# Optimization experiments

Hardware: AMD Instinct MI355X
Metric: run time of the kernel (lower is better)

## Reference

```python
import jax, jax.numpy as jnp
import numpy as np

N_HEAD = 12

def fillnan(x):
    return jnp.nan_to_num(x, nan=0.0, posinf=0.0, neginf=0.0)

def setup_inputs() -> dict:
    key = jax.random.key(0)
    k1, k2, k3 = jax.random.split(key, 3)
    B, T, C = 2, 2048, 768
    x = jax.random.normal(k1, (B, T, C), dtype=jnp.float32)
    W_attn = jax.random.normal(k2, (3 * C, C), dtype=jnp.float32) * 0.02
    W_proj = jax.random.normal(k3, (C, C), dtype=jnp.float32) * 0.02
    return {"x": x, "W_attn": W_attn, "W_proj": W_proj}

def reference(x, W_attn, W_proj):
    B, T, C = x.shape
    H = N_HEAD
    D = C // H
    # qkv projection (torch Linear: x @ W^T), then nan-sanitize
    qkv = fillnan(jnp.einsum('btc,fc->btf', x, W_attn))  # [B,T,3C]
    q, k, v = jnp.split(qkv, 3, axis=-1)
    # [B,T,C] -> [B,H,T,D]
    q = q.reshape(B, T, H, D).transpose(0, 2, 1, 3)
    k = k.reshape(B, T, H, D).transpose(0, 2, 1, 3)
    v = v.reshape(B, T, H, D).transpose(0, 2, 1, 3)
    scale = 1.0 / np.sqrt(D).astype(np.float32)
    att = jnp.einsum('bhqd,bhkd->bhqk', q, k) * scale  # [B,H,T,T]
    att = fillnan(att)
    causal = jnp.tril(jnp.ones((T, T), dtype=bool))
    att = jnp.where(causal[None, None], att, -jnp.inf)
    att = jax.nn.softmax(att, axis=-1)
    att = fillnan(att)
    y = jnp.einsum('bhqk,bhkd->bhqd', att, v)  # [B,H,T,D]
    y = fillnan(y)
    y = y.transpose(0, 2, 1, 3).reshape(B, T, C)
    y = fillnan(jnp.einsum('btc,fc->btf', y, W_proj))
    return y
```

## Files before the change

kernel.cpp:

```cpp
#include <hip/hip_runtime.h>

typedef __attribute__((ext_vector_type(8))) short bf16x8;
typedef __attribute__((ext_vector_type(4))) float f32x4;

__device__ __forceinline__ unsigned short f2b(float f) {
  union { float f; unsigned u; } v; v.f = f;
  return (unsigned short)((v.u + 0x7FFFu + ((v.u >> 16) & 1u)) >> 16);
}
__device__ __forceinline__ unsigned short f2b_fast(float f) {
  union { float f; unsigned u; } v; v.f = f;
  return (unsigned short)((v.u + 0x8000u) >> 16);
}

#define XN4   786432
#define WAN4  442368
#define WPN4  147456
__global__ void cvt_all(const float* __restrict__ x, const float* __restrict__ Wa,
                        const float* __restrict__ Wp,
                        unsigned short* __restrict__ xb, unsigned short* __restrict__ Wab,
                        unsigned short* __restrict__ Wpb) {
  int i = blockIdx.x * 256 + threadIdx.x;
  const float* src; unsigned short* dst; int off;
  if (i < XN4)            { src = x;  dst = xb;  off = i; }
  else if (i < XN4 + WAN4){ src = Wa; dst = Wab; off = i - XN4; }
  else                    { src = Wp; dst = Wpb; off = i - XN4 - WAN4; }
  float4 f = reinterpret_cast<const float4*>(src)[off];
  ushort4 o;
  o.x = f2b(f.x); o.y = f2b(f.y); o.z = f2b(f.z); o.w = f2b(f.w);
  reinterpret_cast<ushort4*>(dst)[off] = o;
}

#define BM 128
#define BN 128
#define BK 64

__global__ __launch_bounds__(256, 2)
void gemm_nt(const unsigned short* __restrict__ A,
             const unsigned short* __restrict__ Bm,
             int M, int N, int K, int mode,
             unsigned short* __restrict__ qb,
             unsigned short* __restrict__ kb_,
             unsigned short* __restrict__ vt,
             float* __restrict__ outf) {
  __shared__ unsigned short As[BM * BK];
  __shared__ unsigned short Bs[BN * BK];
  int tid = threadIdx.x;
  int wave = tid >> 6, lane = tid & 63;
  int quad = lane >> 4, l16 = lane & 15;
  int m0 = blockIdx.x * BM, n0 = blockIdx.y * BN;
  int wm = (wave & 1) * 64, wn = (wave >> 1) * 64;

  int srow = lane >> 3;
  int scol = ((lane & 7) ^ srow) << 3;

  f32x4 acc[4][4] = {};

  for (int k0 = 0; k0 < K; k0 += BK) {
    __syncthreads();
#pragma unroll
    for (int i = 0; i < 4; ++i) {
      int r = wave * 32 + i * 8;
      __builtin_amdgcn_global_load_lds(
          (const __attribute__((address_space(1))) unsigned int*)(A + (size_t)(m0 + r + srow) * K + k0 + scol),
          (__attribute__((address_space(3))) unsigned int*)(As + r * BK), 16, 0, 0);
      __builtin_amdgcn_global_load_lds(
          (const __attribute__((address_space(1))) unsigned int*)(Bm + (size_t)(n0 + r + srow) * K + k0 + scol),
          (__attribute__((address_space(3))) unsigned int*)(Bs + r * BK), 16, 0, 0);
    }
    __syncthreads();
#pragma unroll
    for (int kb = 0; kb < 2; ++kb) {
      int ch = (((kb << 2) | quad) ^ (l16 & 7)) << 3;
      bf16x8 af[4], bf[4];
#pragma unroll
      for (int i = 0; i < 4; ++i)
        af[i] = *reinterpret_cast<const bf16x8*>(As + (wm + i * 16 + l16) * BK + ch);
#pragma unroll
      for (int j = 0; j < 4; ++j)
        bf[j] = *reinterpret_cast<const bf16x8*>(Bs + (wn + j * 16 + l16) * BK + ch);
#pragma unroll
      for (int i = 0; i < 4; ++i)
#pragma unroll
        for (int j = 0; j < 4; ++j)
          acc[i][j] = __builtin_amdgcn_mfma_f32_16x16x32_bf16(af[i], bf[j], acc[i][j], 0, 0, 0);
    }
  }

  const float scale2 = 0.125f * 1.44269504089f;
#pragma unroll
  for (int i = 0; i < 4; ++i) {
    int mbase = m0 + wm + i * 16 + quad * 4;
#pragma unroll
    for (int j = 0; j < 4; ++j) {
      int f = n0 + wn + j * 16 + l16;
#pragma unroll
      for (int r = 0; r < 4; ++r) {
        float c = acc[i][j][r];
        int m = mbase + r;
        if (mode == 0) {
          int b = m >> 11, t = m & 2047;
          int which = f / 768;
          int f2 = f - which * 768;
          int h = f2 >> 6, d = f2 & 63;
          int bh = b * 12 + h;
          if (which == 0)      qb[((size_t)(bh * 2048 + t)) * 64 + d] = f2b(c * scale2);
          else if (which == 1) kb_[((size_t)(bh * 2048 + t)) * 64 + d] = f2b(c);
          else                 vt[((size_t)(bh * 64 + d)) * 2048 + t] = f2b(c);
        } else {
          outf[(size_t)m * N + f] = c;
        }
      }
    }
  }
}

#define PLDP 72

__global__ __launch_bounds__(256, 2)
void attn_part(const unsigned short* __restrict__ Qb,
               const unsigned short* __restrict__ Kb,
               const unsigned short* __restrict__ Vt,
               unsigned short* __restrict__ Yb) {
  __shared__ unsigned short Ks[2][64 * 64];
  __shared__ unsigned short Vs[2][64 * 64];
  __shared__ unsigned short P[4 * 32 * PLDP];
  const int T = 2048, D = 64;
  int wave = threadIdx.x >> 6, lane = threadIdx.x & 63;
  int quad = lane >> 4, l16 = lane & 15;

  int bh = blockIdx.x % 24;
  int qb = 15 - blockIdx.x / 24;
  int q0 = qb * 128;
  int qrow = q0 + wave * 32;
  int nt = 2 * qb + 2;

  const unsigned short* Qp = Qb + (size_t)bh * T * D;
  const unsigned short* Kp = Kb + (size_t)bh * T * D;
  const unsigned short* Vp = Vt + (size_t)bh * D * T;
  unsigned short* Pw = P + wave * 32 * PLDP;

  int srow = lane >> 3;
  int scol = ((lane & 7) ^ srow) << 3;

  bf16x8 aq[2][2];
#pragma unroll
  for (int qi = 0; qi < 2; ++qi)
#pragma unroll
    for (int cc = 0; cc < 2; ++cc)
      aq[qi][cc] = *reinterpret_cast<const bf16x8*>(
          Qp + (qrow + qi * 16 + l16) * D + cc * 32 + quad * 8);

  bf16x8 ones;
#pragma unroll
  for (int e = 0; e < 8; ++e) ones[e] = (short)0x3F80;

  f32x4 o[2][4] = {};
  f32x4 lacc[2] = {};

#define STAGE_KV(buf, k0s)                                                          \
  {                                                                                 \
    _Pragma("unroll")                                                               \
    for (int i_ = 0; i_ < 2; ++i_) {                                                \
      int rr_ = wave * 16 + i_ * 8;                                                 \
      __builtin_amdgcn_global_load_lds(                                             \
          (const __attribute__((address_space(1))) unsigned int*)(Kp + (size_t)((k0s) + rr_ + srow) * 64 + scol), \
          (__attribute__((address_space(3))) unsigned int*)(&Ks[buf][rr_ * 64]), 16, 0, 0); \
      __builtin_amdgcn_global_load_lds(                                             \
          (const __attribute__((address_space(1))) unsigned int*)(Vp + (size_t)(rr_ + srow) * 2048 + (k0s) + scol), \
          (__attribute__((address_space(3))) unsigned int*)(&Vs[buf][rr_ * 64]), 16, 0, 0); \
    }                                                                               \
  }

  STAGE_KV(0, 0);
  asm volatile("s_waitcnt vmcnt(0)" ::: "memory");
  __builtin_amdgcn_s_barrier();

  int cur = 0;
  for (int t = 0; t < nt; ++t) {
    int k0 = t << 6;
    if (t + 1 < nt) STAGE_KV(cur ^ 1, (t + 1) << 6);

    if (k0 <= qrow + 31) {
      f32x4 sacc[2][4] = {};
      __builtin_amdgcn_s_setprio(1);
#pragma unroll
      for (int nt2 = 0; nt2 < 4; ++nt2) {
        bf16x8 bk0 = *reinterpret_cast<const bf16x8*>(Ks[cur] + (nt2 * 16 + l16) * 64 + ((quad ^ (l16 & 7)) << 3));
        bf16x8 bk1 = *reinterpret_cast<const bf16x8*>(Ks[cur] + (nt2 * 16 + l16) * 64 + (((4 | quad) ^ (l16 & 7)) << 3));
#pragma unroll
        for (int qi = 0; qi < 2; ++qi) {
          sacc[qi][nt2] = __builtin_amdgcn_mfma_f32_16x16x32_bf16(aq[qi][0], bk0, sacc[qi][nt2], 0, 0, 0);
          sacc[qi][nt2] = __builtin_amdgcn_mfma_f32_16x16x32_bf16(aq[qi][1], bk1, sacc[qi][nt2], 0, 0, 0);
        }
      }
      __builtin_amdgcn_s_setprio(0);

      if (k0 + 63 > qrow) {
#pragma unroll
        for (int qi = 0; qi < 2; ++qi)
#pragma unroll
          for (int nt2 = 0; nt2 < 4; ++nt2) {
            int col = k0 + nt2 * 16 + l16;
#pragma unroll
            for (int rr = 0; rr < 4; ++rr) {
              int row = qrow + qi * 16 + quad * 4 + rr;
              sacc[qi][nt2][rr] = (col <= row) ? sacc[qi][nt2][rr] : -1e30f;
            }
          }
      }
#pragma unroll
      for (int qi = 0; qi < 2; ++qi)
#pragma unroll
        for (int nt2 = 0; nt2 < 4; ++nt2)
#pragma unroll
          for (int rr = 0; rr < 4; ++rr)
            sacc[qi][nt2][rr] = exp2f(sacc[qi][nt2][rr]);

#pragma unroll
      for (int qi = 0; qi < 2; ++qi)
#pragma unroll
        for (int nt2 = 0; nt2 < 4; ++nt2)
#pragma unroll
          for (int rr = 0; rr < 4; ++rr)
            Pw[(qi * 16 + quad * 4 + rr) * PLDP + nt2 * 16 + l16] = f2b_fast(sacc[qi][nt2][rr]);
      __asm__ volatile("s_waitcnt lgkmcnt(0)" ::: "memory");

      bf16x8 vf[4][2];
#pragma unroll
      for (int dt = 0; dt < 4; ++dt) {
        vf[dt][0] = *reinterpret_cast<const bf16x8*>(Vs[cur] + (dt * 16 + l16) * 64 + ((quad ^ (l16 & 7)) << 3));
        vf[dt][1] = *reinterpret_cast<const bf16x8*>(Vs[cur] + (dt * 16 + l16) * 64 + (((4 | quad) ^ (l16 & 7)) << 3));
      }
      __builtin_amdgcn_s_setprio(1);
#pragma unroll
      for (int qi = 0; qi < 2; ++qi) {
        bf16x8 ap0 = *reinterpret_cast<const bf16x8*>(Pw + (qi * 16 + l16) * PLDP + quad * 8);
        bf16x8 ap1 = *reinterpret_cast<const bf16x8*>(Pw + (qi * 16 + l16) * PLDP + 32 + quad * 8);
#pragma unroll
        for (int dt = 0; dt < 4; ++dt) {
          o[qi][dt] = __builtin_amdgcn_mfma_f32_16x16x32_bf16(ap0, vf[dt][0], o[qi][dt], 0, 0, 0);
          o[qi][dt] = __builtin_amdgcn_mfma_f32_16x16x32_bf16(ap1, vf[dt][1], o[qi][dt], 0, 0, 0);
        }
        lacc[qi] = __builtin_amdgcn_mfma_f32_16x16x32_bf16(ap0, ones, lacc[qi], 0, 0, 0);
        lacc[qi] = __builtin_amdgcn_mfma_f32_16x16x32_bf16(ap1, ones, lacc[qi], 0, 0, 0);
      }
      __builtin_amdgcn_s_setprio(0);
    }

    asm volatile("s_waitcnt vmcnt(0)" ::: "memory");
    __builtin_amdgcn_s_barrier();
    cur ^= 1;
  }

  int b = bh / 12, h = bh - b * 12;
  unsigned short* Yw = Yb + (size_t)b * 2048 * 768 + h * 64;
#pragma unroll
  for (int qi = 0; qi < 2; ++qi)
#pragma unroll
    for (int rr = 0; rr < 4; ++rr) {
      int row = qrow + qi * 16 + quad * 4 + rr;
      float rl = 1.0f / lacc[qi][rr];
#pragma unroll
      for (int dt = 0; dt < 4; ++dt)
        Yw[(size_t)row * 768 + dt * 16 + l16] = f2b(o[qi][dt][rr] * rl);
    }
}

extern "C" void kernel_launch(void* const* d_in, const int* in_sizes, int n_in,
                              void* d_out, int out_size, void* d_ws, size_t ws_size,
                              hipStream_t stream) {
  const float* x  = (const float*)d_in[0];
  const float* Wa = (const float*)d_in[1];
  const float* Wp = (const float*)d_in[2];
  float* out = (float*)d_out;

  unsigned short* ws = (unsigned short*)d_ws;
  unsigned short* xb  = ws;
  unsigned short* Wab = xb  + 3145728;
  unsigned short* Wpb = Wab + 1769472;
  unsigned short* Qb  = Wpb + 589824;
  unsigned short* Kb  = Qb  + 3145728;
  unsigned short* Vt  = Kb  + 3145728;
  unsigned short* Yb  = Vt  + 3145728;

  cvt_all<<<(XN4 + WAN4 + WPN4) / 256, 256, 0, stream>>>(x, Wa, Wp, xb, Wab, Wpb);

  gemm_nt<<<dim3(4096 / BM, 2304 / BN), 256, 0, stream>>>(
      xb, Wab, 4096, 2304, 768, 0, Qb, Kb, Vt, nullptr);

  attn_part<<<384, 256, 0, stream>>>(Qb, Kb, Vt, Yb);

  gemm_nt<<<dim3(4096 / BM, 768 / BN), 256, 0, stream>>>(
      Yb, Wpb, 4096, 768, 768, 1, nullptr, nullptr, nullptr, out);
}
```

Before: 166.2 us.

## Split causal attention along KV into balanced chunks with separate combine kernel

Each query block's KV range is now split into a number of chunks that grows with its causal length, so the grid goes from 384 to 960 more evenly sized blocks. Partial unnormalized outputs and row sums are written to fp32 workspace, and a new combine kernel sums them and normalizes into bf16 Y. Occupancy hint is raised to 3 blocks per CU. The aim is less tail imbalance from the causal triangle and better CU fill; the cost is extra fp32 partial-output traffic and one more kernel launch. Summing partials without rescaling assumes the softmax uses no per-row running max, which appears to hold in the existing code.

```diff
diff --git a/kernel.cpp b/kernel.cpp
--- a/kernel.cpp
+++ b/kernel.cpp
@@ -116,11 +116,11 @@
 
 #define PLDP 72
 
-__global__ __launch_bounds__(256, 2)
+__global__ __launch_bounds__(256, 3)
 void attn_part(const unsigned short* __restrict__ Qb,
                const unsigned short* __restrict__ Kb,
                const unsigned short* __restrict__ Vt,
-               unsigned short* __restrict__ Yb) {
+               float* __restrict__ Opart, float* __restrict__ Lpart) {
   __shared__ unsigned short Ks[2][64 * 64];
   __shared__ unsigned short Vs[2][64 * 64];
   __shared__ unsigned short P[4 * 32 * PLDP];
@@ -128,11 +128,20 @@
   int wave = threadIdx.x >> 6, lane = threadIdx.x & 63;
   int quad = lane >> 4, l16 = lane & 15;
 
-  int bh = blockIdx.x % 24;
-  int qb = 15 - blockIdx.x / 24;
+  int w = blockIdx.x;
+  int bh = w / 40;
+  int r = 39 - (w - bh * 40);
+  int qb, ci;
+  if (r < 4)       { qb = r;                 ci = 0; }
+  else if (r < 12) { qb = 4 + ((r - 4) >> 1);  ci = (r - 4) & 1; }
+  else if (r < 24) { qb = 8 + (r - 12) / 3;    ci = (r - 12) % 3; }
+  else             { qb = 12 + ((r - 24) >> 2); ci = (r - 24) & 3; }
+  int nk = 2 * qb + 2;
+  int nc = (qb >> 2) + 1;
+  int t0 = ci * nk / nc, t1 = (ci + 1) * nk / nc;
+
   int q0 = qb * 128;
   int qrow = q0 + wave * 32;
-  int nt = 2 * qb + 2;
 
   const unsigned short* Qp = Qb + (size_t)bh * T * D;
   const unsigned short* Kp = Kb + (size_t)bh * T * D;
@@ -171,14 +180,14 @@
     }                                                                               \
   }
 
-  STAGE_KV(0, 0);
+  STAGE_KV(0, t0 << 6);
   asm volatile("s_waitcnt vmcnt(0)" ::: "memory");
   __builtin_amdgcn_s_barrier();
 
   int cur = 0;
-  for (int t = 0; t < nt; ++t) {
+  for (int t = t0; t < t1; ++t) {
     int k0 = t << 6;
-    if (t + 1 < nt) STAGE_KV(cur ^ 1, (t + 1) << 6);
+    if (t + 1 < t1) STAGE_KV(cur ^ 1, (t + 1) << 6);
 
     if (k0 <= qrow + 31) {
       f32x4 sacc[2][4] = {};
@@ -252,18 +261,51 @@
     cur ^= 1;
   }
 
+  float* Op = Opart + (size_t)blockIdx.x * 8192 + wave * 32 * 64;
+#pragma unroll
+  for (int qi = 0; qi < 2; ++qi)
+#pragma unroll
+    for (int dt = 0; dt < 4; ++dt)
+#pragma unroll
+      for (int rr = 0; rr < 4; ++rr)
+        Op[(qi * 16 + quad * 4 + rr) * 64 + dt * 16 + l16] = o[qi][dt][rr];
+  if (l16 == 0) {
+#pragma unroll
+    for (int qi = 0; qi < 2; ++qi)
+#pragma unroll
+      for (int rr = 0; rr < 4; ++rr)
+        Lpart[blockIdx.x * 128 + wave * 32 + qi * 16 + quad * 4 + rr] = lacc[qi][rr];
+  }
+}
+
+__global__ __launch_bounds__(256)
+void attn_combine(const float* __restrict__ Opart, const float* __restrict__ Lpart,
+                  unsigned short* __restrict__ Yb) {
+  int blk = blockIdx.x;
+  int bh = blk >> 4, qb = blk & 15;
+  int off = (qb < 4) ? qb : (qb < 8) ? 4 + 2 * (qb - 4)
+          : (qb < 12) ? 12 + 3 * (qb - 8) : 24 + 4 * (qb - 12);
+  int nc = (qb >> 2) + 1;
   int b = bh / 12, h = bh - b * 12;
-  unsigned short* Yw = Yb + (size_t)b * 2048 * 768 + h * 64;
-#pragma unroll
-  for (int qi = 0; qi < 2; ++qi)
-#pragma unroll
-    for (int rr = 0; rr < 4; ++rr) {
-      int row = qrow + qi * 16 + quad * 4 + rr;
-      float rl = 1.0f / lacc[qi][rr];
-#pragma unroll
-      for (int dt = 0; dt < 4; ++dt)
-        Yw[(size_t)row * 768 + dt * 16 + l16] = f2b(o[qi][dt][rr] * rl);
-    }
+  int q0 = qb * 128;
+#pragma unroll
+  for (int i = 0; i < 8; ++i) {
+    int idx = i * 256 + threadIdx.x;
+    int row = idx >> 4, c4 = idx & 15;
+    float4 s = {0.f, 0.f, 0.f, 0.f};
+    float L = 0.f;
+    for (int ci = 0; ci < nc; ++ci) {
+      size_t pb = (size_t)(bh * 40 + 39 - (off + ci));
+      float4 v = *reinterpret_cast<const float4*>(Opart + pb * 8192 + row * 64 + c4 * 4);
+      s.x += v.x; s.y += v.y; s.z += v.z; s.w += v.w;
+      L += Lpart[pb * 128 + row];
+    }
+    float rl = 1.0f / L;
+    ushort4 y;
+    y.x = f2b(s.x * rl); y.y = f2b(s.y * rl);
+    y.z = f2b(s.z * rl); y.w = f2b(s.w * rl);
+    *reinterpret_cast<ushort4*>(Yb + ((size_t)(b * 2048 + q0 + row)) * 768 + h * 64 + c4 * 4) = y;
+  }
 }
 
 extern "C" void kernel_launch(void* const* d_in, const int* in_sizes, int n_in,
@@ -282,13 +324,16 @@
   unsigned short* Kb  = Qb  + 3145728;
   unsigned short* Vt  = Kb  + 3145728;
   unsigned short* Yb  = Vt  + 3145728;
+  float*          Opart = (float*)(Yb + 3145728);
+  float*          Lpart = Opart + 7864320;
 
   cvt_all<<<(XN4 + WAN4 + WPN4) / 256, 256, 0, stream>>>(x, Wa, Wp, xb, Wab, Wpb);
 
   gemm_nt<<<dim3(4096 / BM, 2304 / BN), 256, 0, stream>>>(
       xb, Wab, 4096, 2304, 768, 0, Qb, Kb, Vt, nullptr);
 
-  attn_part<<<384, 256, 0, stream>>>(Qb, Kb, Vt, Yb);
+  attn_part<<<960, 256, 0, stream>>>(Qb, Kb, Vt, Opart, Lpart);
+  attn_combine<<<384, 256, 0, stream>>>(Opart, Lpart, Yb);
 
   gemm_nt<<<dim3(4096 / BM, 768 / BN), 256, 0, stream>>>(
       Yb, Wpb, 4096, 768, 768, 1, nullptr, nullptr, nullptr, out);
```

Result: no change. 163.6 us (-1.5%).
